# Kernel tuning notes

Hardware: AMD Instinct MI355X
Metric: run time of the kernel (lower is better)

The kernel has to match this reference:

```python
import jax, jax.numpy as jnp
import numpy as np

B, L, D, H = 16, 512, 1024, 16
DH = D // H
NEG = -1e9  # stands in for -inf mask fill (same softmax result, grad-safe)


def setup_inputs() -> dict:
    key = jax.random.key(0)
    ks = jax.random.split(key, 8)
    x = jax.random.normal(ks[0], (B, L, D), dtype=jnp.float32)
    mask = jnp.ones((B, L), dtype=jnp.int64)
    qmask = jax.random.randint(ks[1], (B, L), 0, 9).astype(jnp.int64)
    # qkv_linear: Linear(D, 4D, bias=False); store as [D, 4D] so y = x @ Wqkv
    Wqkv = jax.random.normal(ks[2], (D, 4 * D), dtype=jnp.float32) / np.sqrt(D)
    # fc: Linear(D, D) with bias; store as [D, D] so y = x @ Wfc + bfc
    Wfc = jax.random.normal(ks[3], (D, D), dtype=jnp.float32) / np.sqrt(D)
    bfc = jnp.zeros((D,), dtype=jnp.float32)
    shift = jnp.abs(jax.random.normal(ks[4], (1,), dtype=jnp.float32)) + 0.001
    bias_p = -jnp.abs(jax.random.normal(ks[5], (1,), dtype=jnp.float32))
    return {"x": x, "mask": mask, "qmask": qmask, "Wqkv": Wqkv,
            "Wfc": Wfc, "bfc": bfc, "shift": shift, "bias_p": bias_p,
            "use_Gaussian": 1}


def reference(x, mask, qmask, Wqkv, Wfc, bfc, shift, bias_p, use_Gaussian):
    b, l, d = x.shape
    qkv = x @ Wqkv                                  # [B, L, 4D]
    q, k1, k2, v = jnp.split(qkv, 4, axis=-1)
    q = q.reshape(b, l, H, DH)                      # [B, L, H, dh]
    k1 = k1.reshape(b, l, H, DH)
    k2 = k2.reshape(b, l, H, DH)
    v = v.reshape(b, l, H, DH)

    attn_self = jnp.einsum('bqhd,bkhd->bhqk', q, k1)    # [B, H, L, L]
    attn_others = jnp.einsum('bqhd,bkhd->bhqk', q, k2)  # [B, H, L, L]

    same = (qmask[:, :, None] == qmask[:, None, :])[:, None]  # [B, 1, L, L]
    attn = jnp.where(same, attn_self, attn_others)  # scale == 1 (scale=False)

    key_valid = (mask != 0)[:, None, None, :]       # [B, 1, 1, L]
    attn = jnp.where(key_valid, attn, NEG)

    if use_Gaussian:
        idx = jnp.arange(l, dtype=jnp.float32)
        sq_dist = (idx[:, None] - idx[None, :]) ** 2        # [L, L]
        dis = -(shift[0] * sq_dist + bias_p[0])
        attn = attn + dis[None, None]

    attn = jax.nn.softmax(attn, axis=-1)            # dropout: eval mode (no-op)
    out = jnp.einsum('bhqk,bkhd->bqhd', attn, v).reshape(b, l, d)
    return out @ Wfc + bfc
```

## Files before the change

kernel.cpp:

```cpp
#include <hip/hip_runtime.h>
#include <hip/hip_bf16.h>

#define B_  16
#define L_  512
#define D_  1024
#define H_  16
#define DH_ 64
#define NEG_ (-1e9f)
#define QB2 32
#define KB2 32
#define LDP 72

#define GK  1024
#define NT  32

typedef unsigned short ushort_t;
typedef __attribute__((ext_vector_type(8))) short bf16x8;
typedef __attribute__((ext_vector_type(4))) float f32x4;

__device__ __forceinline__ ushort_t f2bf(float f) {
    unsigned u = __float_as_uint(f);
    u += 0x7FFFu + ((u >> 16) & 1u);
    return (ushort_t)(u >> 16);
}
__device__ __forceinline__ unsigned packbf(float a, float b) {
    return (unsigned)f2bf(a) | ((unsigned)f2bf(b) << 16);
}

__device__ __forceinline__ void gload_lds16(const void* g, void* l) {
    __builtin_amdgcn_global_load_lds(
        (const __attribute__((address_space(1))) void*)g,
        (__attribute__((address_space(3))) void*)l, 16, 0, 0);
}

__global__ __launch_bounds__(256) void prep_all(const float* __restrict__ x,
                                                const float* __restrict__ Wqkv,
                                                const float* __restrict__ Wfc,
                                                ushort_t* __restrict__ xbf,
                                                ushort_t* __restrict__ WqT,
                                                ushort_t* __restrict__ WfT) {
    __shared__ float tile[32][33];
    const int bid = blockIdx.x;
    const int t   = threadIdx.x;

    if (bid < 8192) {
        const int i = (bid * 256 + t) * 4;
        const float4 v = *(const float4*)&x[i];
        ushort4 o;
        o.x = f2bf(v.x); o.y = f2bf(v.y); o.z = f2bf(v.z); o.w = f2bf(v.w);
        *(ushort4*)&xbf[i] = o;
        return;
    }
    const float* src; ushort_t* dst; int C, gx, gy;
    if (bid < 8192 + 4096) {
        const int lb = bid - 8192;
        src = Wqkv; dst = WqT; C = 4096; gx = lb & 127; gy = lb >> 7;
    } else {
        const int lb = bid - 12288;
        src = Wfc;  dst = WfT; C = 1024; gx = lb & 31;  gy = lb >> 5;
    }
    const int R  = 1024;
    const int r0 = gy * 32, c0 = gx * 32;
    const int tr = t >> 3, tc = (t & 7) * 4;
    const float4 v = *(const float4*)&src[(size_t)(r0 + tr) * C + c0 + tc];
    tile[tr][tc + 0] = v.x;
    tile[tr][tc + 1] = v.y;
    tile[tr][tc + 2] = v.z;
    tile[tr][tc + 3] = v.w;
    __syncthreads();
    ushort4 o;
    o.x = f2bf(tile[tc + 0][tr]);
    o.y = f2bf(tile[tc + 1][tr]);
    o.z = f2bf(tile[tc + 2][tr]);
    o.w = f2bf(tile[tc + 3][tr]);
    *(ushort4*)&dst[(size_t)(c0 + tr) * R + r0 + tc] = o;
}

__global__ __launch_bounds__(256) void gemm_bf16_mfma(const ushort_t* __restrict__ A,
                                                      const ushort_t* __restrict__ Bt,
                                                      const float* __restrict__ bias,
                                                      float* __restrict__ C,
                                                      int M, int N, int K) {
    __shared__ __align__(16) ushort_t As[128 * 64];
    __shared__ __align__(16) ushort_t Bs[128 * 64];

    const int t    = threadIdx.x;
    const int wave = t >> 6;
    const int lane = t & 63;
    const int m0   = blockIdx.y * 128;
    const int n0   = blockIdx.x * 128;
    const int wr   = wave >> 1;
    const int wc   = wave & 1;

    const int lrow = lane >> 3;
    const int ksl  = (lane & 7) ^ lrow;
    const int llo  = lane & 15;
    const int lhi  = lane >> 4;

    f32x4 acc[4][4] = {};

    for (int k0 = 0; k0 < K; k0 += 64) {
        #pragma unroll
        for (int i = 0; i < 4; ++i) {
            const int row = wave * 32 + i * 8;
            gload_lds16(A + (size_t)(m0 + row + lrow) * K + k0 + ksl * 8,
                        As + (size_t)row * 64);
            gload_lds16(Bt + (size_t)(n0 + row + lrow) * K + k0 + ksl * 8,
                        Bs + (size_t)row * 64);
        }
        __syncthreads();

        #pragma unroll
        for (int ks = 0; ks < 2; ++ks) {
            bf16x8 af[4], bfr[4];
            #pragma unroll
            for (int m = 0; m < 4; ++m) {
                const int row = wr * 64 + m * 16 + llo;
                af[m] = *(const bf16x8*)&As[row * 64 + (((ks * 4 + lhi) ^ (row & 7)) << 3)];
            }
            #pragma unroll
            for (int n = 0; n < 4; ++n) {
                const int row = wc * 64 + n * 16 + llo;
                bfr[n] = *(const bf16x8*)&Bs[row * 64 + (((ks * 4 + lhi) ^ (row & 7)) << 3)];
            }
            #pragma unroll
            for (int m = 0; m < 4; ++m)
                #pragma unroll
                for (int n = 0; n < 4; ++n)
                    acc[m][n] = __builtin_amdgcn_mfma_f32_16x16x32_bf16(
                        af[m], bfr[n], acc[m][n], 0, 0, 0);
        }
        __syncthreads();
    }

    #pragma unroll
    for (int m = 0; m < 4; ++m) {
        #pragma unroll
        for (int n = 0; n < 4; ++n) {
            const int col = n0 + wc * 64 + n * 16 + llo;
            const float bv = bias[col];
            #pragma unroll
            for (int i = 0; i < 4; ++i) {
                const int row = m0 + wr * 64 + m * 16 + lhi * 4 + i;
                C[(size_t)row * N + col] = acc[m][n][i] + bv;
            }
        }
    }
}

__device__ __forceinline__ bf16x8 frag_ld(const ushort_t* tile, int row, int lhi) {
    const int slot = lhi ^ ((row >> 1) & 3);
    return *(const bf16x8*)&tile[row * 32 + (slot << 3)];
}

__global__ __launch_bounds__(512, 2) void gemm256_8p(const ushort_t* __restrict__ A,
                                                     const ushort_t* __restrict__ Bt,
                                                     ushort_t* __restrict__ C,
                                                     int nbn, int N) {
    extern __shared__ __align__(16) ushort_t lds[];

    const int t    = threadIdx.x;
    const int wave = t >> 6;
    const int lane = t & 63;
    const int wr   = wave >> 2;
    const int wc   = wave & 3;
    const int lhi  = lane >> 4;
    const int llo  = lane & 15;
    const int srow  = lane >> 2;
    const int sslot = (lane & 3) ^ ((lane >> 3) & 3);

    const int cpx = gridDim.x >> 3;
    const int swz = (blockIdx.x & 7) * cpx + (blockIdx.x >> 3);
    const int m0  = (swz / nbn) * 256;
    const int n0  = (swz % nbn) * 256;

    #define STAGE_H(mat, gptr, grow0, kt, half)                                         \
        gload_lds16((gptr) + (size_t)((grow0) + (half) * 128 + (wave << 4) + srow) * GK \
                        + (kt) * 32 + (sslot << 3),                                     \
                    lds + ((((kt) & 3) * 2 + (mat)) * 8192                              \
                           + ((half) * 128 + (wave << 4)) * 32))

    f32x4 acc[8][4] = {};

    STAGE_H(0, A,  m0, 0, 0); STAGE_H(0, A,  m0, 0, 1);
    STAGE_H(1, Bt, n0, 0, 0); STAGE_H(1, Bt, n0, 0, 1);
    STAGE_H(0, A,  m0, 1, 0); STAGE_H(0, A,  m0, 1, 1);
    STAGE_H(1, Bt, n0, 1, 0); STAGE_H(1, Bt, n0, 1, 1);
    asm volatile("s_waitcnt vmcnt(4)" ::: "memory");
    __builtin_amdgcn_s_barrier();

    for (int kt = 0; kt < NT; ++kt) {
        const ushort_t* At  = lds + ((kt & 3) * 2 + 0) * 8192;
        const ushort_t* Bti = lds + ((kt & 3) * 2 + 1) * 8192;

        bf16x8 afr[4], bfr[4];

        #pragma unroll
        for (int n = 0; n < 4; ++n)
            bfr[n] = frag_ld(Bti, wc * 64 + n * 16 + llo, lhi);
        #pragma unroll
        for (int mi = 0; mi < 4; ++mi)
            afr[mi] = frag_ld(At, wr * 128 + mi * 16 + llo, lhi);
        if (kt + 2 < NT) {
            STAGE_H(0, A, m0, kt + 2, 0);
            STAGE_H(0, A, m0, kt + 2, 1);
        }
        __builtin_amdgcn_s_setprio(1);
        #pragma unroll
        for (int mi = 0; mi < 4; ++mi)
            #pragma unroll
            for (int n = 0; n < 4; ++n)
                acc[mi][n] = __builtin_amdgcn_mfma_f32_16x16x32_bf16(
                    afr[mi], bfr[n], acc[mi][n], 0, 0, 0);
        __builtin_amdgcn_s_setprio(0);

        #pragma unroll
        for (int mi = 0; mi < 4; ++mi)
            afr[mi] = frag_ld(At, wr * 128 + (mi + 4) * 16 + llo, lhi);
        if (kt + 2 < NT) {
            STAGE_H(1, Bt, n0, kt + 2, 0);
            STAGE_H(1, Bt, n0, kt + 2, 1);
        }
        __builtin_amdgcn_s_setprio(1);
        #pragma unroll
        for (int mi = 0; mi < 4; ++mi)
            #pragma unroll
            for (int n = 0; n < 4; ++n)
                acc[mi + 4][n] = __builtin_amdgcn_mfma_f32_16x16x32_bf16(
                    afr[mi], bfr[n], acc[mi + 4][n], 0, 0, 0);
        __builtin_amdgcn_s_setprio(0);

        if (kt + 2 < NT)      { asm volatile("s_waitcnt vmcnt(4)" ::: "memory"); }
        else if (kt + 1 < NT) { asm volatile("s_waitcnt vmcnt(0)" ::: "memory"); }
        __builtin_amdgcn_s_barrier();
    }
    #undef STAGE_H

    #pragma unroll
    for (int mi = 0; mi < 8; ++mi) {
        #pragma unroll
        for (int n = 0; n < 4; ++n) {
            const int col = n0 + wc * 64 + n * 16 + llo;
            #pragma unroll
            for (int i = 0; i < 4; ++i) {
                const int row = m0 + wr * 128 + mi * 16 + lhi * 4 + i;
                C[(size_t)row * N + col] = f2bf(acc[mi][n][i]);
            }
        }
    }
}

__global__ __launch_bounds__(128) void attn_mfma(const ushort_t* __restrict__ qkv,
                                                 const int* __restrict__ mask,
                                                 const int* __restrict__ qmask,
                                                 const float* __restrict__ shiftp,
                                                 const float* __restrict__ biasp,
                                                 const int* __restrict__ useg,
                                                 ushort_t* __restrict__ O) {
    __shared__ __align__(16) ushort_t K1s[KB2][LDP];
    __shared__ __align__(16) ushort_t K2s[KB2][LDP];
    __shared__ __align__(16) ushort_t Vt[DH_][36];
    __shared__ __align__(16) unsigned Ps32[QB2][36];
    __shared__ __align__(16) int      Ms[L_];

    const int t    = threadIdx.x;
    const int wave = t >> 6;
    const int lane = t & 63;
    const int lhi  = lane >> 4;
    const int llo  = lane & 15;

    const int orig = blockIdx.x;
    const int swz  = (orig & 7) * 512 + (orig >> 3);
    const int bh   = swz >> 4;
    const int qb   = swz & 15;
    const int b    = bh >> 4;
    const int h    = bh & 15;
    const int q0   = qb * QB2;

    const float shiftv = shiftp[0];
    const float biasv  = biasp[0];
    const int   useG   = useg[0];
    const size_t rowbase = (size_t)b * L_ * (4 * D_);
    const int    hoff    = h * DH_;

    int lo = 0, hi = (L_ / KB2) - 1;
    if (useG) {
        while (lo < hi) {
            const int k0 = lo * KB2;
            int dmin = (k0 > q0) ? (k0 - (q0 + QB2 - 1)) : (q0 - (k0 + KB2 - 1));
            if (dmin < 0) dmin = 0;
            if (shiftv * (float)dmin * (float)dmin > 240.f) ++lo; else break;
        }
        while (hi > lo) {
            const int k0 = hi * KB2;
            int dmin = (k0 > q0) ? (k0 - (q0 + QB2 - 1)) : (q0 - (k0 + KB2 - 1));
            if (dmin < 0) dmin = 0;
            if (shiftv * (float)dmin * (float)dmin > 240.f) --hi; else break;
        }
    }

    for (int k = lo * KB2 + t; k < (hi + 1) * KB2; k += 128)
        Ms[k] = (qmask[b * L_ + k] << 1) | (mask[b * L_ + k] != 0 ? 1 : 0);

    const int gq = q0 + wave * 16 + llo;
    bf16x8 af_q[2];
    #pragma unroll
    for (int ks = 0; ks < 2; ++ks)
        af_q[ks] = *(const bf16x8*)&qkv[rowbase + (size_t)gq * (4 * D_) + hoff
                                        + ks * 32 + lhi * 8];
    const int qm_q = qmask[b * L_ + gq];

    float m_run = -1e30f, l_run = 0.f;
    f32x4 acc_o[4] = {};

    const int srow = t >> 2;
    const int scol = (t & 3) * 8;
    const int vkv  = t & 31;
    const int vd0  = (t >> 5) * 8;

    uint4 pk1[2], pk2[2], pvv[2];

    #define ISSUE_KV(kt_) do {                                                          \
        const int k0_ = (kt_) * KB2;                                                    \
        _Pragma("unroll")                                                               \
        for (int it = 0; it < 2; ++it) {                                                \
            const size_t gb = rowbase + (size_t)(k0_ + srow) * (4 * D_) + hoff          \
                              + scol + it * 32;                                         \
            pk1[it] = *(const uint4*)&qkv[gb + D_];                                     \
            pk2[it] = *(const uint4*)&qkv[gb + 2 * D_];                                 \
            pvv[it] = *(const uint4*)&qkv[rowbase + (size_t)(k0_ + vkv) * (4 * D_)      \
                                          + 3 * D_ + hoff + vd0 + it * 32];             \
        }                                                                               \
    } while (0)

    ISSUE_KV(lo);

    for (int kt = lo; kt <= hi; ++kt) {
        const int k0 = kt * KB2;

        #pragma unroll
        for (int it = 0; it < 2; ++it) {
            *(uint4*)&K1s[srow][scol + it * 32] = pk1[it];
            *(uint4*)&K2s[srow][scol + it * 32] = pk2[it];
            const int d = vd0 + it * 32;
            const uint4 raw = pvv[it];
            Vt[d + 0][vkv] = (ushort_t)(raw.x & 0xFFFFu);
            Vt[d + 1][vkv] = (ushort_t)(raw.x >> 16);
            Vt[d + 2][vkv] = (ushort_t)(raw.y & 0xFFFFu);
            Vt[d + 3][vkv] = (ushort_t)(raw.y >> 16);
            Vt[d + 4][vkv] = (ushort_t)(raw.z & 0xFFFFu);
            Vt[d + 5][vkv] = (ushort_t)(raw.z >> 16);
            Vt[d + 6][vkv] = (ushort_t)(raw.w & 0xFFFFu);
            Vt[d + 7][vkv] = (ushort_t)(raw.w >> 16);
        }
        if (kt < hi) ISSUE_KV(kt + 1);
        __syncthreads();

        f32x4 s1[2], s2[2];
        #pragma unroll
        for (int n = 0; n < 2; ++n) { s1[n] = (f32x4){0,0,0,0}; s2[n] = (f32x4){0,0,0,0}; }
        #pragma unroll
        for (int ks = 0; ks < 2; ++ks) {
            const int kb = ks * 32 + lhi * 8;
            #pragma unroll
            for (int n = 0; n < 2; ++n) {
                const bf16x8 bk1 = *(const bf16x8*)&K1s[n * 16 + llo][kb];
                const bf16x8 bk2 = *(const bf16x8*)&K2s[n * 16 + llo][kb];
                s1[n] = __builtin_amdgcn_mfma_f32_16x16x32_bf16(bk1, af_q[ks], s1[n], 0, 0, 0);
                s2[n] = __builtin_amdgcn_mfma_f32_16x16x32_bf16(bk2, af_q[ks], s2[n], 0, 0, 0);
            }
        }

        float sv[2][4];
        float mx = -1e30f;
        #pragma unroll
        for (int n = 0; n < 2; ++n) {
            const int4 mc = *(const int4*)&Ms[k0 + n * 16 + lhi * 4];
            const int mci[4] = {mc.x, mc.y, mc.z, mc.w};
            #pragma unroll
            for (int i = 0; i < 4; ++i) {
                const int key = k0 + n * 16 + lhi * 4 + i;
                float x = ((mci[i] >> 1) == qm_q) ? s1[n][i] : s2[n][i];
                if (!(mci[i] & 1)) x = NEG_;
                if (useG) {
                    const float dq = (float)(gq - key);
                    x -= shiftv * dq * dq + biasv;
                }
                sv[n][i] = x;
                mx = fmaxf(mx, x);
            }
        }
        mx = fmaxf(mx, __shfl_xor(mx, 16));
        mx = fmaxf(mx, __shfl_xor(mx, 32));

        const float m_new = fmaxf(m_run, mx);
        const float scale = __expf(m_run - m_new);

        float p[2][4], ls = 0.f;
        #pragma unroll
        for (int n = 0; n < 2; ++n)
            #pragma unroll
            for (int i = 0; i < 4; ++i) {
                p[n][i] = __expf(sv[n][i] - m_new);
                ls += p[n][i];
            }
        ls += __shfl_xor(ls, 16);
        ls += __shfl_xor(ls, 32);
        l_run = l_run * scale + ls;
        m_run = m_new;

        #pragma unroll
        for (int n2 = 0; n2 < 4; ++n2) {
            acc_o[n2][0] *= scale; acc_o[n2][1] *= scale;
            acc_o[n2][2] *= scale; acc_o[n2][3] *= scale;
        }

        const int qrow = wave * 16 + llo;
        #pragma unroll
        for (int n = 0; n < 2; ++n) {
            uint2 w;
            w.x = packbf(p[n][0], p[n][1]);
            w.y = packbf(p[n][2], p[n][3]);
            *(uint2*)&Ps32[qrow][n * 8 + lhi * 2] = w;
        }

        {
            const int kb = lhi * 8;
            const bf16x8 bp = *(const bf16x8*)&Ps32[qrow][lhi * 4];
            #pragma unroll
            for (int n2 = 0; n2 < 4; ++n2) {
                const bf16x8 av = *(const bf16x8*)&Vt[n2 * 16 + llo][kb];
                acc_o[n2] = __builtin_amdgcn_mfma_f32_16x16x32_bf16(av, bp, acc_o[n2], 0, 0, 0);
            }
        }
        __syncthreads();
    }
    #undef ISSUE_KV

    {
        const float inv = 1.f / l_run;
        const int qrow = wave * 16 + llo;
        #pragma unroll
        for (int n2 = 0; n2 < 4; ++n2) {
            uint2 w;
            w.x = packbf(acc_o[n2][0] * inv, acc_o[n2][1] * inv);
            w.y = packbf(acc_o[n2][2] * inv, acc_o[n2][3] * inv);
            *(uint2*)&Ps32[qrow][n2 * 8 + lhi * 2] = w;
        }
    }
    __syncthreads();
    {
        const int row = t >> 2;
        const int c4  = (t & 3) * 8;
        const uint4 a  = *(const uint4*)&Ps32[row][c4];
        const uint4 b2 = *(const uint4*)&Ps32[row][c4 + 4];
        ushort_t* dst = &O[(size_t)(b * L_ + q0 + row) * D_ + hoff + c4 * 2];
        *(uint4*)dst       = a;
        *(uint4*)(dst + 8) = b2;
    }
}

extern "C" void kernel_launch(void* const* d_in, const int* in_sizes, int n_in,
                              void* d_out, int out_size, void* d_ws, size_t ws_size,
                              hipStream_t stream) {
    const float* x      = (const float*)d_in[0];
    const int*   mask   = (const int*)d_in[1];
    const int*   qmask  = (const int*)d_in[2];
    const float* Wqkv   = (const float*)d_in[3];
    const float* Wfc    = (const float*)d_in[4];
    const float* bfc    = (const float*)d_in[5];
    const float* shift  = (const float*)d_in[6];
    const float* bias_p = (const float*)d_in[7];
    const int*   useg   = (const int*)d_in[8];
    float*       out    = (float*)d_out;

    const int M  = B_ * L_;
    const int N1 = 4 * D_;

    ushort_t* qkv = (ushort_t*)d_ws;
    ushort_t* Obf = qkv + (size_t)M * N1;
    ushort_t* xbf = Obf + (size_t)M * D_;
    ushort_t* WqT = xbf + (size_t)M * D_;
    ushort_t* WfT = WqT + (size_t)N1 * D_;

    prep_all<<<dim3(8192 + 4096 + 1024), 256, 0, stream>>>(x, Wqkv, Wfc,
                                                           xbf, WqT, WfT);

    gemm256_8p<<<dim3((M / 256) * (N1 / 256)), 512, 131072, stream>>>(
        xbf, WqT, qkv, N1 / 256, N1);

    attn_mfma<<<dim3((B_ * H_) * (L_ / QB2)), 128, 0, stream>>>(qkv, mask, qmask,
                                                                shift, bias_p, useg, Obf);

    gemm_bf16_mfma<<<dim3(D_ / 128, M / 128), 256, 0, stream>>>(
        Obf, WfT, bfc, out, M, D_, D_);
}
```

Measured before the change: 159.9 us.

## Shrink QKV GEMM to 128x128 tiles with triple-buffered LDS pipeline

Replaces the 256x256-tile, 8-wave QKV projection GEMM with a 128x128-tile, 4-wave kernel using a 3-stage LDS ring (48 KB) instead of a 4-slot 128 KB ring. It launches four times as many blocks and allows three blocks per CU, aiming for better occupancy and latency hiding. The cost is lower arithmetic intensity per block: each tile is reused less, so global and LDS traffic per FLOP goes up.

```diff
diff --git a/kernel.cpp b/kernel.cpp
--- a/kernel.cpp
+++ b/kernel.cpp
@@ -153,7 +153,7 @@
     return *(const bf16x8*)&tile[row * 32 + (slot << 3)];
 }
 
-__global__ __launch_bounds__(512, 2) void gemm256_8p(const ushort_t* __restrict__ A,
+__global__ __launch_bounds__(256, 3) void gemm128_fr(const ushort_t* __restrict__ A,
                                                      const ushort_t* __restrict__ Bt,
                                                      ushort_t* __restrict__ C,
                                                      int nbn, int N) {
@@ -162,8 +162,8 @@
     const int t    = threadIdx.x;
     const int wave = t >> 6;
     const int lane = t & 63;
-    const int wr   = wave >> 2;
-    const int wc   = wave & 3;
+    const int wr   = wave >> 1;
+    const int wc   = wave & 1;
     const int lhi  = lane >> 4;
     const int llo  = lane & 15;
     const int srow  = lane >> 2;
@@ -171,40 +171,44 @@
 
     const int cpx = gridDim.x >> 3;
     const int swz = (blockIdx.x & 7) * cpx + (blockIdx.x >> 3);
-    const int m0  = (swz / nbn) * 256;
-    const int n0  = (swz % nbn) * 256;
-
-    #define STAGE_H(mat, gptr, grow0, kt, half)                                         \
-        gload_lds16((gptr) + (size_t)((grow0) + (half) * 128 + (wave << 4) + srow) * GK \
-                        + (kt) * 32 + (sslot << 3),                                     \
-                    lds + ((((kt) & 3) * 2 + (mat)) * 8192                              \
-                           + ((half) * 128 + (wave << 4)) * 32))
-
-    f32x4 acc[8][4] = {};
-
-    STAGE_H(0, A,  m0, 0, 0); STAGE_H(0, A,  m0, 0, 1);
-    STAGE_H(1, Bt, n0, 0, 0); STAGE_H(1, Bt, n0, 0, 1);
-    STAGE_H(0, A,  m0, 1, 0); STAGE_H(0, A,  m0, 1, 1);
-    STAGE_H(1, Bt, n0, 1, 0); STAGE_H(1, Bt, n0, 1, 1);
+    const int m0  = (swz / nbn) * 128;
+    const int n0  = (swz % nbn) * 128;
+
+    #define STAGE_T(mat, gptr, g0, kt, buf)                                        \
+        _Pragma("unroll")                                                          \
+        for (int j = 0; j < 2; ++j) {                                              \
+            gload_lds16((gptr) + (size_t)((g0) + j * 64 + (wave << 4) + srow) * GK \
+                            + (kt) * 32 + (sslot << 3),                            \
+                        lds + ((buf) * 2 + (mat)) * 4096                           \
+                            + (j * 64 + (wave << 4)) * 32);                        \
+        }
+
+    f32x4 acc[4][4] = {};
+
+    STAGE_T(0, A,  m0, 0, 0); STAGE_T(1, Bt, n0, 0, 0);
+    STAGE_T(0, A,  m0, 1, 1); STAGE_T(1, Bt, n0, 1, 1);
     asm volatile("s_waitcnt vmcnt(4)" ::: "memory");
     __builtin_amdgcn_s_barrier();
 
     for (int kt = 0; kt < NT; ++kt) {
-        const ushort_t* At  = lds + ((kt & 3) * 2 + 0) * 8192;
-        const ushort_t* Bti = lds + ((kt & 3) * 2 + 1) * 8192;
+        const int buf = kt % 3;
+        const ushort_t* Ab = lds + (buf * 2 + 0) * 4096;
+        const ushort_t* Bb = lds + (buf * 2 + 1) * 4096;
 
         bf16x8 afr[4], bfr[4];
-
+        #pragma unroll
+        for (int mi = 0; mi < 4; ++mi)
+            afr[mi] = frag_ld(Ab, wr * 64 + mi * 16 + llo, lhi);
         #pragma unroll
         for (int n = 0; n < 4; ++n)
-            bfr[n] = frag_ld(Bti, wc * 64 + n * 16 + llo, lhi);
-        #pragma unroll
-        for (int mi = 0; mi < 4; ++mi)
-            afr[mi] = frag_ld(At, wr * 128 + mi * 16 + llo, lhi);
+            bfr[n] = frag_ld(Bb, wc * 64 + n * 16 + llo, lhi);
+
         if (kt + 2 < NT) {
-            STAGE_H(0, A, m0, kt + 2, 0);
-            STAGE_H(0, A, m0, kt + 2, 1);
-        }
+            const int nb = (kt + 2) % 3;
+            STAGE_T(0, A,  m0, kt + 2, nb);
+            STAGE_T(1, Bt, n0, kt + 2, nb);
+        }
+
         __builtin_amdgcn_s_setprio(1);
         #pragma unroll
         for (int mi = 0; mi < 4; ++mi)
@@ -214,36 +218,20 @@
                     afr[mi], bfr[n], acc[mi][n], 0, 0, 0);
         __builtin_amdgcn_s_setprio(0);
 
-        #pragma unroll
-        for (int mi = 0; mi < 4; ++mi)
-            afr[mi] = frag_ld(At, wr * 128 + (mi + 4) * 16 + llo, lhi);
-        if (kt + 2 < NT) {
-            STAGE_H(1, Bt, n0, kt + 2, 0);
-            STAGE_H(1, Bt, n0, kt + 2, 1);
-        }
-        __builtin_amdgcn_s_setprio(1);
-        #pragma unroll
-        for (int mi = 0; mi < 4; ++mi)
-            #pragma unroll
-            for (int n = 0; n < 4; ++n)
-                acc[mi + 4][n] = __builtin_amdgcn_mfma_f32_16x16x32_bf16(
-                    afr[mi], bfr[n], acc[mi + 4][n], 0, 0, 0);
-        __builtin_amdgcn_s_setprio(0);
-
         if (kt + 2 < NT)      { asm volatile("s_waitcnt vmcnt(4)" ::: "memory"); }
         else if (kt + 1 < NT) { asm volatile("s_waitcnt vmcnt(0)" ::: "memory"); }
         __builtin_amdgcn_s_barrier();
     }
-    #undef STAGE_H
+    #undef STAGE_T
 
     #pragma unroll
-    for (int mi = 0; mi < 8; ++mi) {
+    for (int mi = 0; mi < 4; ++mi) {
         #pragma unroll
         for (int n = 0; n < 4; ++n) {
             const int col = n0 + wc * 64 + n * 16 + llo;
             #pragma unroll
             for (int i = 0; i < 4; ++i) {
-                const int row = m0 + wr * 128 + mi * 16 + lhi * 4 + i;
+                const int row = m0 + wr * 64 + mi * 16 + lhi * 4 + i;
                 C[(size_t)row * N + col] = f2bf(acc[mi][n][i]);
             }
         }
@@ -486,8 +474,8 @@
     prep_all<<<dim3(8192 + 4096 + 1024), 256, 0, stream>>>(x, Wqkv, Wfc,
                                                            xbf, WqT, WfT);
 
-    gemm256_8p<<<dim3((M / 256) * (N1 / 256)), 512, 131072, stream>>>(
-        xbf, WqT, qkv, N1 / 256, N1);
+    gemm128_fr<<<dim3((M / 128) * (N1 / 128)), 256, 49152, stream>>>(
+        xbf, WqT, qkv, N1 / 128, N1);
 
     attn_mfma<<<dim3((B_ * H_) * (L_ / QB2)), 128, 0, stream>>>(qkv, mask, qmask,
                                                                 shift, bias_p, useg, Obf);
```

Result: slower. 178.7 us (+11.7%).
